# Optimization experiments

Measured on AMD Instinct MI355X. Metric: run time of the kernel, lower is better.

## Reference

```python
import jax, jax.numpy as jnp
import numpy as np
from jax import lax

S = 1024   # max_num_segments
CB = 25    # color_hist_bins
TB = 10    # texture_hist_bins
EPS = 1e-12


def setup_inputs() -> dict:
    key = jax.random.key(0)
    k1, k2, k3, k4 = jax.random.split(key, 4)
    B, C, R, H, W = 8, 3, 8, 512, 512
    img = jax.random.normal(k1, (B, C, H, W), jnp.float32)
    imgs_bins = jax.random.randint(k2, (B, C, H, W), 0, CB, jnp.int32)
    grads_bins = jax.random.randint(k3, (B, C, R, H, W), 0, TB, jnp.int32)
    reg_lab = jax.random.randint(k4, (B, H, W), 0, S, jnp.int32)
    return {"img": img, "imgs_bins": imgs_bins, "grads_bins": grads_bins, "reg_lab": reg_lab}


def reference(img, imgs_bins, grads_bins, reg_lab):
    B, C, H, W = img.shape
    R = grads_bins.shape[2]
    HW = H * W
    lab = reg_lab.astype(jnp.int32)

    # ---- area_per_segment: scatter_add of ones over flattened labels ----
    flat = (lab.reshape(B, HW) + (jnp.arange(B, dtype=jnp.int32) * S)[:, None]).reshape(-1)
    area = jnp.zeros(B * S, jnp.int32).at[flat].add(1).reshape(B, S)

    # ---- bbox_per_segment: scatter amin/amax of pixel coordinates ----
    yy, xx = jnp.meshgrid(jnp.arange(H, dtype=jnp.int32),
                          jnp.arange(W, dtype=jnp.int32), indexing='ij')
    xb = jnp.broadcast_to(xx.reshape(HW), (B, HW)).reshape(-1)
    yb = jnp.broadcast_to(yy.reshape(HW), (B, HW)).reshape(-1)
    xmin = jnp.full(B * S, W, jnp.int32).at[flat].min(xb)
    ymin = jnp.full(B * S, H, jnp.int32).at[flat].min(yb)
    xmax = jnp.zeros(B * S, jnp.int32).at[flat].max(xb)
    ymax = jnp.zeros(B * S, jnp.int32).at[flat].max(yb)
    # torch does xywh[2:] -= xywh[:2] (no +1), so w = xmax - xmin
    bbox_xywh = jnp.stack([xmin, ymin, xmax - xmin, ymax - ymin], -1).reshape(B, S, 4)

    area_f = area.astype(jnp.float32)

    # ---- color histogram: scatter_add of ones into [B,C,S*CB] ----
    ci = (lab[:, None, :, :] * CB + imgs_bins).reshape(B * C, HW)
    ci = (ci + (jnp.arange(B * C, dtype=jnp.int32) * (S * CB))[:, None]).reshape(-1)
    color_hist = jnp.zeros(B * C * S * CB, jnp.float32).at[ci].add(1.0).reshape(B, C, S, CB)
    color_hist = color_hist.transpose(0, 2, 1, 3).reshape(B, S, C * CB)  # [B,S,C*CB]
    color_hist = color_hist / (area_f * float(C) + EPS)[..., None]

    # ---- texture histogram: scatter_add of ones into [B,C,R,S*TB] ----
    ti = (lab[:, None, None, :, :] * TB + grads_bins).reshape(B * C * R, HW)
    ti = (ti + (jnp.arange(B * C * R, dtype=jnp.int32) * (S * TB))[:, None]).reshape(-1)
    texture_hist = jnp.zeros(B * C * R * S * TB, jnp.float32).at[ti].add(1.0).reshape(B, C, R, S, TB)
    texture_hist = texture_hist.transpose(0, 3, 1, 2, 4).reshape(B, S, C * R * TB)  # [B,S,C*R*TB]
    texture_hist = texture_hist / (area_f * float(C * R) + EPS)[..., None]

    # ---- image_scharr_gradients: depthwise-style conv2d, padding=1 ----
    sx = jnp.array([[-3., 0., 3.], [-10., 0., 10.], [-3., 0., 3.]], jnp.float32)
    kern = jnp.stack([sx, sx.T])[:, None]  # [2,1,3,3]
    grads = lax.conv_general_dilated(img.reshape(B * C, 1, H, W), kern, (1, 1), 'SAME',
                                     dimension_numbers=('NCHW', 'OIHW', 'NCHW'))
    grads = grads.reshape(B, C, 2, H, W)

    return area, bbox_xywh, color_hist, texture_hist, grads
```

## Files before the change

kernel.cpp:

```cpp
#include <hip/hip_runtime.h>

#define B_ 8
#define C_ 3
#define R_ 8
#define H_ 512
#define W_ 512
#define HW_ (H_*W_)
#define S_ 1024
#define CB_ 25
#define TB_ 10

#define O_AREA 0
#define O_BBOX 8192
#define O_COLOR 40960
#define O_TEX 655360
#define O_GRADS 2621440

#define NBBOX 8
#define NTEX (B_*C_*R_)
#define NCOL (B_*C_)
#define NHIST (NBBOX + NTEX + NCOL)
#define NCONV 1024
#define NGRID (NHIST + NCONV)

__global__ __launch_bounds__(1024) void k_fused(
    const float* __restrict__ img,
    const int* __restrict__ imgs_bins,
    const int* __restrict__ grads_bins,
    const int* __restrict__ lab,
    float* __restrict__ out) {
  __shared__ unsigned smem[12800];
  const int bid = blockIdx.x;
  const int tid = threadIdx.x;

  if (bid < NBBOX) {
    const int b = bid;
    int* mn = (int*)smem;
    for (int i = tid; i < S_; i += 1024) {
      mn[i] = W_; mn[S_ + i] = H_; mn[2*S_ + i] = 0; mn[3*S_ + i] = 0;
    }
    __syncthreads();
    const int4* lp = (const int4*)(lab + (size_t)b * HW_);
    for (int t = tid; t < HW_/4; t += 1024) {
      const int4 lv = lp[t];
      const int p = t * 4;
      const int y = p >> 9;
      const int x = p & (W_ - 1);
      atomicMin(&mn[lv.x], x);       atomicMin(&mn[S_ + lv.x], y);
      atomicMax(&mn[2*S_ + lv.x], x);   atomicMax(&mn[3*S_ + lv.x], y);
      atomicMin(&mn[lv.y], x + 1);   atomicMin(&mn[S_ + lv.y], y);
      atomicMax(&mn[2*S_ + lv.y], x + 1); atomicMax(&mn[3*S_ + lv.y], y);
      atomicMin(&mn[lv.z], x + 2);   atomicMin(&mn[S_ + lv.z], y);
      atomicMax(&mn[2*S_ + lv.z], x + 2); atomicMax(&mn[3*S_ + lv.z], y);
      atomicMin(&mn[lv.w], x + 3);   atomicMin(&mn[S_ + lv.w], y);
      atomicMax(&mn[2*S_ + lv.w], x + 3); atomicMax(&mn[3*S_ + lv.w], y);
    }
    __syncthreads();
    {
      const int xmn = mn[tid], ymn = mn[S_ + tid];
      const int xmx = mn[2*S_ + tid], ymx = mn[3*S_ + tid];
      float4 v;
      v.x = (float)xmn; v.y = (float)ymn;
      v.z = (float)(xmx - xmn); v.w = (float)(ymx - ymn);
      ((float4*)(out + O_BBOX))[b * S_ + tid] = v;
    }
  } else if (bid < NBBOX + NTEX) {
    const int plane = bid - NBBOX;
    const int b = plane / (C_*R_);
    const int cr = plane - b * (C_*R_);
    int* h = (int*)smem;
    for (int i = tid; i < S_*TB_; i += 1024) h[i] = 0;
    __syncthreads();
    const int4* bp = (const int4*)(grads_bins + (size_t)plane * HW_);
    const int4* lp = (const int4*)(lab + (size_t)b * HW_);
    for (int t = tid; t < HW_/4; t += 1024) {
      const int4 bn = bp[t];
      const int4 lv = lp[t];
      atomicAdd(&h[lv.x*TB_ + bn.x], 1);
      atomicAdd(&h[lv.y*TB_ + bn.y], 1);
      atomicAdd(&h[lv.z*TB_ + bn.z], 1);
      atomicAdd(&h[lv.w*TB_ + bn.w], 1);
    }
    __syncthreads();
    {
      const int base = tid * TB_;
      int s = 0;
      #pragma unroll
      for (int t = 0; t < TB_; ++t) s += h[base + t];
      const float inv = 1.0f / ((float)s * 24.0f + 1e-12f);
      float* o = out + O_TEX + (size_t)b * (S_ * C_*R_*TB_) + tid * (C_*R_*TB_) + cr * TB_;
      #pragma unroll
      for (int t = 0; t < TB_; ++t) o[t] = (float)h[base + t] * inv;
      if (cr == 0) out[O_AREA + b * S_ + tid] = (float)s;
    }
  } else if (bid < NHIST) {
    const int plane = bid - NBBOX - NTEX;
    const int b = plane / C_;
    const int c = plane - b * C_;
    unsigned* h = smem;
    for (int i = tid; i < (S_*CB_)/2; i += 1024) h[i] = 0;
    __syncthreads();
    const int4* bp = (const int4*)(imgs_bins + (size_t)plane * HW_);
    const int4* lp = (const int4*)(lab + (size_t)b * HW_);
    for (int t = tid; t < HW_/4; t += 1024) {
      const int4 bn = bp[t];
      const int4 lv = lp[t];
      const int j0 = lv.x*CB_ + bn.x;
      const int j1 = lv.y*CB_ + bn.y;
      const int j2 = lv.z*CB_ + bn.z;
      const int j3 = lv.w*CB_ + bn.w;
      atomicAdd(&h[j0 >> 1], 1u << ((j0 & 1) << 4));
      atomicAdd(&h[j1 >> 1], 1u << ((j1 & 1) << 4));
      atomicAdd(&h[j2 >> 1], 1u << ((j2 & 1) << 4));
      atomicAdd(&h[j3 >> 1], 1u << ((j3 & 1) << 4));
    }
    __syncthreads();
    {
      int s = 0;
      #pragma unroll
      for (int ci = 0; ci < CB_; ++ci) {
        const int j = tid * CB_ + ci;
        s += (int)((h[j >> 1] >> ((j & 1) << 4)) & 0xFFFFu);
      }
      const float inv = 1.0f / ((float)s * 3.0f + 1e-12f);
      float* o = out + O_COLOR + (size_t)b * (S_ * C_*CB_) + tid * (C_*CB_) + c * CB_;
      #pragma unroll
      for (int ci = 0; ci < CB_; ++ci) {
        const int j = tid * CB_ + ci;
        o[ci] = (float)((h[j >> 1] >> ((j & 1) << 4)) & 0xFFFFu) * inv;
      }
    }
  } else {
    const int cb = bid - NHIST;
    const int tot = B_*C_*HW_;
    for (int i = cb * 1024 + tid; i < tot; i += NCONV * 1024) {
      const int pix = i & (HW_ - 1);
      const int bc = i >> 18;
      const int x = pix & (W_ - 1);
      const int y = pix >> 9;
      const float* im = img + (size_t)bc * HW_;
      const bool xm = x > 0, xp = x < W_ - 1, ym = y > 0, yp = y < H_ - 1;
      const float i00 = (ym && xm) ? im[pix - W_ - 1] : 0.f;
      const float i01 = ym ? im[pix - W_] : 0.f;
      const float i02 = (ym && xp) ? im[pix - W_ + 1] : 0.f;
      const float i10 = xm ? im[pix - 1] : 0.f;
      const float i12 = xp ? im[pix + 1] : 0.f;
      const float i20 = (yp && xm) ? im[pix + W_ - 1] : 0.f;
      const float i21 = yp ? im[pix + W_] : 0.f;
      const float i22 = (yp && xp) ? im[pix + W_ + 1] : 0.f;
      const float gx = 3.f*(i02 - i00) + 10.f*(i12 - i10) + 3.f*(i22 - i20);
      const float gy = 3.f*(i20 - i00) + 10.f*(i21 - i01) + 3.f*(i22 - i02);
      out[O_GRADS + (size_t)(bc*2 + 0)*HW_ + pix] = gx;
      out[O_GRADS + (size_t)(bc*2 + 1)*HW_ + pix] = gy;
    }
  }
}

extern "C" void kernel_launch(void* const* d_in, const int* in_sizes, int n_in,
                              void* d_out, int out_size, void* d_ws, size_t ws_size,
                              hipStream_t stream) {
  const float* img = (const float*)d_in[0];
  const int* imgs_bins = (const int*)d_in[1];
  const int* grads_bins = (const int*)d_in[2];
  const int* reg_lab = (const int*)d_in[3];
  float* out = (float*)d_out;

  hipLaunchKernelGGL(k_fused, dim3(NGRID), dim3(1024), 0, stream,
                     img, imgs_bins, grads_bins, reg_lab, out);
}
```

Measured before the change: 78.12 us.

## Split histogram planes into chunks with scratch partials and separate reduce kernel

```diff
diff --git a/kernel.cpp b/kernel.cpp
--- a/kernel.cpp
+++ b/kernel.cpp
@@ -16,64 +16,69 @@
 #define O_TEX 655360
 #define O_GRADS 2621440
 
-#define NBBOX 8
-#define NTEX (B_*C_*R_)
-#define NCOL (B_*C_)
-#define NHIST (NBBOX + NTEX + NCOL)
-#define NCONV 1024
-#define NGRID (NHIST + NCONV)
-
-__global__ __launch_bounds__(1024) void k_fused(
+#define NTEX 768
+#define NCOL 96
+#define NBB  128
+#define NAREA 8
+#define NHIST (NTEX + NCOL + NBB + NAREA)
+#define NCONV 512
+#define NGRID1 (NHIST + NCONV)
+
+#define SC_TEX 0
+#define SC_COL (NTEX * 5120)
+#define SC_B   (SC_COL + NCOL * 12800)
+#define SCR_WORDS (SC_B + NBB * 2048)
+#define NEED_WS ((size_t)SCR_WORDS * 4)
+
+#define T_TEX (B_*C_*R_*S_*TB_)
+#define T_COL (B_*C_*S_*CB_)
+#define T_BB  (B_*S_)
+#define NGRID2 ((T_TEX + T_COL + T_BB) / 1024)
+
+__device__ __forceinline__ void conv_px(const float* __restrict__ img,
+                                        float* __restrict__ out, int i) {
+  const int pix = i & (HW_ - 1);
+  const int bc = i >> 18;
+  const int x = pix & (W_ - 1);
+  const int y = pix >> 9;
+  const float* im = img + (size_t)bc * HW_;
+  const bool xm = x > 0, xp = x < W_ - 1, ym = y > 0, yp = y < H_ - 1;
+  const float i00 = (ym && xm) ? im[pix - W_ - 1] : 0.f;
+  const float i01 = ym ? im[pix - W_] : 0.f;
+  const float i02 = (ym && xp) ? im[pix - W_ + 1] : 0.f;
+  const float i10 = xm ? im[pix - 1] : 0.f;
+  const float i12 = xp ? im[pix + 1] : 0.f;
+  const float i20 = (yp && xm) ? im[pix + W_ - 1] : 0.f;
+  const float i21 = yp ? im[pix + W_] : 0.f;
+  const float i22 = (yp && xp) ? im[pix + W_ + 1] : 0.f;
+  const float gx = 3.f*(i02 - i00) + 10.f*(i12 - i10) + 3.f*(i22 - i20);
+  const float gy = 3.f*(i20 - i00) + 10.f*(i21 - i01) + 3.f*(i22 - i02);
+  out[O_GRADS + (size_t)(bc*2 + 0)*HW_ + pix] = gx;
+  out[O_GRADS + (size_t)(bc*2 + 1)*HW_ + pix] = gy;
+}
+
+__global__ __launch_bounds__(1024) void k_part(
     const float* __restrict__ img,
     const int* __restrict__ imgs_bins,
     const int* __restrict__ grads_bins,
     const int* __restrict__ lab,
-    float* __restrict__ out) {
+    float* __restrict__ out,
+    unsigned* __restrict__ scr,
+    int pxsplit) {
   __shared__ unsigned smem[12800];
   const int bid = blockIdx.x;
   const int tid = threadIdx.x;
 
-  if (bid < NBBOX) {
-    const int b = bid;
-    int* mn = (int*)smem;
-    for (int i = tid; i < S_; i += 1024) {
-      mn[i] = W_; mn[S_ + i] = H_; mn[2*S_ + i] = 0; mn[3*S_ + i] = 0;
-    }
-    __syncthreads();
-    const int4* lp = (const int4*)(lab + (size_t)b * HW_);
-    for (int t = tid; t < HW_/4; t += 1024) {
-      const int4 lv = lp[t];
-      const int p = t * 4;
-      const int y = p >> 9;
-      const int x = p & (W_ - 1);
-      atomicMin(&mn[lv.x], x);       atomicMin(&mn[S_ + lv.x], y);
-      atomicMax(&mn[2*S_ + lv.x], x);   atomicMax(&mn[3*S_ + lv.x], y);
-      atomicMin(&mn[lv.y], x + 1);   atomicMin(&mn[S_ + lv.y], y);
-      atomicMax(&mn[2*S_ + lv.y], x + 1); atomicMax(&mn[3*S_ + lv.y], y);
-      atomicMin(&mn[lv.z], x + 2);   atomicMin(&mn[S_ + lv.z], y);
-      atomicMax(&mn[2*S_ + lv.z], x + 2); atomicMax(&mn[3*S_ + lv.z], y);
-      atomicMin(&mn[lv.w], x + 3);   atomicMin(&mn[S_ + lv.w], y);
-      atomicMax(&mn[2*S_ + lv.w], x + 3); atomicMax(&mn[3*S_ + lv.w], y);
-    }
-    __syncthreads();
-    {
-      const int xmn = mn[tid], ymn = mn[S_ + tid];
-      const int xmx = mn[2*S_ + tid], ymx = mn[3*S_ + tid];
-      float4 v;
-      v.x = (float)xmn; v.y = (float)ymn;
-      v.z = (float)(xmx - xmn); v.w = (float)(ymx - ymn);
-      ((float4*)(out + O_BBOX))[b * S_ + tid] = v;
-    }
-  } else if (bid < NBBOX + NTEX) {
-    const int plane = bid - NBBOX;
+  if (bid < NTEX) {
+    const int plane = bid >> 2, chunk = bid & 3;
     const int b = plane / (C_*R_);
-    const int cr = plane - b * (C_*R_);
     int* h = (int*)smem;
     for (int i = tid; i < S_*TB_; i += 1024) h[i] = 0;
     __syncthreads();
-    const int4* bp = (const int4*)(grads_bins + (size_t)plane * HW_);
-    const int4* lp = (const int4*)(lab + (size_t)b * HW_);
-    for (int t = tid; t < HW_/4; t += 1024) {
+    const int4* bp = (const int4*)(grads_bins + (size_t)plane*HW_) + chunk*16384;
+    const int4* lp = (const int4*)(lab + (size_t)b*HW_) + chunk*16384;
+    #pragma unroll 4
+    for (int t = tid; t < 16384; t += 1024) {
       const int4 bn = bp[t];
       const int4 lv = lp[t];
       atomicAdd(&h[lv.x*TB_ + bn.x], 1);
@@ -82,27 +87,23 @@
       atomicAdd(&h[lv.w*TB_ + bn.w], 1);
     }
     __syncthreads();
-    {
-      const int base = tid * TB_;
-      int s = 0;
-      #pragma unroll
-      for (int t = 0; t < TB_; ++t) s += h[base + t];
-      const float inv = 1.0f / ((float)s * 24.0f + 1e-12f);
-      float* o = out + O_TEX + (size_t)b * (S_ * C_*R_*TB_) + tid * (C_*R_*TB_) + cr * TB_;
-      #pragma unroll
-      for (int t = 0; t < TB_; ++t) o[t] = (float)h[base + t] * inv;
-      if (cr == 0) out[O_AREA + b * S_ + tid] = (float)s;
-    }
-  } else if (bid < NHIST) {
-    const int plane = bid - NBBOX - NTEX;
+    unsigned* dst = scr + SC_TEX + (size_t)bid * 5120;
+    const int2* h2 = (const int2*)h;
+    for (int i = tid; i < 5120; i += 1024) {
+      const int2 v = h2[i];
+      dst[i] = (unsigned)v.x | ((unsigned)v.y << 16);
+    }
+  } else if (bid < NTEX + NCOL) {
+    const int rid = bid - NTEX;
+    const int plane = rid >> 2, chunk = rid & 3;
     const int b = plane / C_;
-    const int c = plane - b * C_;
     unsigned* h = smem;
-    for (int i = tid; i < (S_*CB_)/2; i += 1024) h[i] = 0;
-    __syncthreads();
-    const int4* bp = (const int4*)(imgs_bins + (size_t)plane * HW_);
-    const int4* lp = (const int4*)(lab + (size_t)b * HW_);
-    for (int t = tid; t < HW_/4; t += 1024) {
+    for (int i = tid; i < 12800; i += 1024) h[i] = 0;
+    __syncthreads();
+    const int4* bp = (const int4*)(imgs_bins + (size_t)plane*HW_) + chunk*16384;
+    const int4* lp = (const int4*)(lab + (size_t)b*HW_) + chunk*16384;
+    #pragma unroll 4
+    for (int t = tid; t < 16384; t += 1024) {
       const int4 bn = bp[t];
       const int4 lv = lp[t];
       const int j0 = lv.x*CB_ + bn.x;
@@ -115,45 +116,114 @@
       atomicAdd(&h[j3 >> 1], 1u << ((j3 & 1) << 4));
     }
     __syncthreads();
-    {
-      int s = 0;
-      #pragma unroll
-      for (int ci = 0; ci < CB_; ++ci) {
-        const int j = tid * CB_ + ci;
-        s += (int)((h[j >> 1] >> ((j & 1) << 4)) & 0xFFFFu);
-      }
-      const float inv = 1.0f / ((float)s * 3.0f + 1e-12f);
-      float* o = out + O_COLOR + (size_t)b * (S_ * C_*CB_) + tid * (C_*CB_) + c * CB_;
-      #pragma unroll
-      for (int ci = 0; ci < CB_; ++ci) {
-        const int j = tid * CB_ + ci;
-        o[ci] = (float)((h[j >> 1] >> ((j & 1) << 4)) & 0xFFFFu) * inv;
-      }
-    }
+    unsigned* dst = scr + SC_COL + (size_t)rid * 12800;
+    for (int i = tid; i < 12800; i += 1024) dst[i] = h[i];
+  } else if (bid < NTEX + NCOL + NBB) {
+    const int rid = bid - NTEX - NCOL;
+    const int b = rid >> 4, chunk = rid & 15;
+    int* mn = (int*)smem;
+    for (int i = tid; i < 2048; i += 1024) mn[i] = 512;
+    for (int i = tid; i < 2048; i += 1024) mn[2048 + i] = 0;
+    __syncthreads();
+    const int base = chunk * 16384;
+    const int4* lp = (const int4*)(lab + (size_t)b*HW_) + chunk*4096;
+    #pragma unroll 2
+    for (int t = tid; t < 4096; t += 1024) {
+      const int4 lv = lp[t];
+      const int p = base + t*4;
+      const int y = p >> 9;
+      const int x = p & (W_ - 1);
+      atomicMin(&mn[lv.x], x);       atomicMin(&mn[1024 + lv.x], y);
+      atomicMax(&mn[2048 + lv.x], x);     atomicMax(&mn[3072 + lv.x], y);
+      atomicMin(&mn[lv.y], x + 1);   atomicMin(&mn[1024 + lv.y], y);
+      atomicMax(&mn[2048 + lv.y], x + 1); atomicMax(&mn[3072 + lv.y], y);
+      atomicMin(&mn[lv.z], x + 2);   atomicMin(&mn[1024 + lv.z], y);
+      atomicMax(&mn[2048 + lv.z], x + 2); atomicMax(&mn[3072 + lv.z], y);
+      atomicMin(&mn[lv.w], x + 3);   atomicMin(&mn[1024 + lv.w], y);
+      atomicMax(&mn[2048 + lv.w], x + 3); atomicMax(&mn[3072 + lv.w], y);
+    }
+    __syncthreads();
+    unsigned* dst = scr + SC_B + (size_t)rid * 2048;
+    dst[tid]        = (unsigned)mn[tid]        | ((unsigned)mn[1024 + tid] << 16);
+    dst[1024 + tid] = (unsigned)mn[2048 + tid] | ((unsigned)mn[3072 + tid] << 16);
+  } else if (bid < NHIST) {
+    const int b = bid - NTEX - NCOL - NBB;
+    int* cnt = (int*)smem;
+    cnt[tid] = 0;
+    __syncthreads();
+    const int4* lp = (const int4*)(lab + (size_t)b*HW_);
+    #pragma unroll 4
+    for (int t = tid; t < HW_/4; t += 1024) {
+      const int4 lv = lp[t];
+      atomicAdd(&cnt[lv.x], 1);
+      atomicAdd(&cnt[lv.y], 1);
+      atomicAdd(&cnt[lv.z], 1);
+      atomicAdd(&cnt[lv.w], 1);
+    }
+    __syncthreads();
+    out[O_AREA + b*S_ + tid] = (float)cnt[tid];
   } else {
     const int cb = bid - NHIST;
-    const int tot = B_*C_*HW_;
-    for (int i = cb * 1024 + tid; i < tot; i += NCONV * 1024) {
-      const int pix = i & (HW_ - 1);
-      const int bc = i >> 18;
-      const int x = pix & (W_ - 1);
-      const int y = pix >> 9;
-      const float* im = img + (size_t)bc * HW_;
-      const bool xm = x > 0, xp = x < W_ - 1, ym = y > 0, yp = y < H_ - 1;
-      const float i00 = (ym && xm) ? im[pix - W_ - 1] : 0.f;
-      const float i01 = ym ? im[pix - W_] : 0.f;
-      const float i02 = (ym && xp) ? im[pix - W_ + 1] : 0.f;
-      const float i10 = xm ? im[pix - 1] : 0.f;
-      const float i12 = xp ? im[pix + 1] : 0.f;
-      const float i20 = (yp && xm) ? im[pix + W_ - 1] : 0.f;
-      const float i21 = yp ? im[pix + W_] : 0.f;
-      const float i22 = (yp && xp) ? im[pix + W_ + 1] : 0.f;
-      const float gx = 3.f*(i02 - i00) + 10.f*(i12 - i10) + 3.f*(i22 - i20);
-      const float gy = 3.f*(i20 - i00) + 10.f*(i21 - i01) + 3.f*(i22 - i02);
-      out[O_GRADS + (size_t)(bc*2 + 0)*HW_ + pix] = gx;
-      out[O_GRADS + (size_t)(bc*2 + 1)*HW_ + pix] = gy;
-    }
+    for (int i = pxsplit + cb*1024 + tid; i < B_*C_*HW_; i += NCONV*1024)
+      conv_px(img, out, i);
   }
+}
+
+__global__ __launch_bounds__(1024) void k_reduce(float* __restrict__ out,
+                                                 const unsigned* __restrict__ scr) {
+  const int idx = blockIdx.x * 1024 + threadIdx.x;
+  if (idx < T_TEX) {
+    const int b = idx / 245760;
+    const int r1 = idx - b * 245760;
+    const int l = r1 / 240;
+    const int r2 = r1 - l * 240;
+    const int cr = r2 / 10;
+    const int t = r2 - cr * 10;
+    const int j = l * TB_ + t;
+    const unsigned sh = (j & 1) << 4;
+    const unsigned* p = scr + SC_TEX + (size_t)(b*(C_*R_) + cr) * 4 * 5120 + (j >> 1);
+    const unsigned s = ((p[0] >> sh) & 0xFFFFu) + ((p[5120] >> sh) & 0xFFFFu)
+                     + ((p[2*5120] >> sh) & 0xFFFFu) + ((p[3*5120] >> sh) & 0xFFFFu);
+    const float a = out[O_AREA + b*S_ + l];
+    out[O_TEX + idx] = (float)s / (a * 24.0f + 1e-12f);
+  } else if (idx < T_TEX + T_COL) {
+    const int o = idx - T_TEX;
+    const int b = o / 76800;
+    const int r1 = o - b * 76800;
+    const int l = r1 / 75;
+    const int r2 = r1 - l * 75;
+    const int c = r2 / 25;
+    const int ci = r2 - c * 25;
+    const int j = l * CB_ + ci;
+    const unsigned sh = (j & 1) << 4;
+    const unsigned* p = scr + SC_COL + (size_t)(b*C_ + c) * 4 * 12800 + (j >> 1);
+    const unsigned s = ((p[0] >> sh) & 0xFFFFu) + ((p[12800] >> sh) & 0xFFFFu)
+                     + ((p[2*12800] >> sh) & 0xFFFFu) + ((p[3*12800] >> sh) & 0xFFFFu);
+    const float a = out[O_AREA + b*S_ + l];
+    out[O_COLOR + o] = (float)s / (a * 3.0f + 1e-12f);
+  } else {
+    const int i = idx - T_TEX - T_COL;
+    const int b = i >> 10, l = i & (S_ - 1);
+    int xmn = W_, ymn = H_, xmx = 0, ymx = 0;
+    const unsigned* p = scr + SC_B + (size_t)(b*16) * 2048 + l;
+    #pragma unroll
+    for (int k = 0; k < 16; ++k) {
+      const unsigned w0 = p[k*2048];
+      const unsigned w1 = p[k*2048 + 1024];
+      xmn = min(xmn, (int)(w0 & 0xFFFFu)); ymn = min(ymn, (int)(w0 >> 16));
+      xmx = max(xmx, (int)(w1 & 0xFFFFu)); ymx = max(ymx, (int)(w1 >> 16));
+    }
+    float4 v;
+    v.x = (float)xmn; v.y = (float)ymn;
+    v.z = (float)(xmx - xmn); v.w = (float)(ymx - ymn);
+    ((float4*)(out + O_BBOX))[i] = v;
+  }
+}
+
+__global__ __launch_bounds__(1024) void k_conv_lo(const float* __restrict__ img,
+                                                  float* __restrict__ out, int pxsplit) {
+  for (int i = blockIdx.x*1024 + threadIdx.x; i < pxsplit; i += NCONV*1024)
+    conv_px(img, out, i);
 }
 
 extern "C" void kernel_launch(void* const* d_in, const int* in_sizes, int n_in,
@@ -165,6 +235,15 @@
   const int* reg_lab = (const int*)d_in[3];
   float* out = (float*)d_out;
 
-  hipLaunchKernelGGL(k_fused, dim3(NGRID), dim3(1024), 0, stream,
-                     img, imgs_bins, grads_bins, reg_lab, out);
-}
+  const bool ws_ok = ws_size >= NEED_WS;
+  unsigned* scr = ws_ok ? (unsigned*)d_ws : (unsigned*)(out + O_GRADS);
+  const int pxsplit = ws_ok ? 0 : 11 * HW_;
+
+  hipLaunchKernelGGL(k_part, dim3(NGRID1), dim3(1024), 0, stream,
+                     img, imgs_bins, grads_bins, reg_lab, out, scr, pxsplit);
+  hipLaunchKernelGGL(k_reduce, dim3(NGRID2), dim3(1024), 0, stream, out, scr);
+  if (!ws_ok) {
+    hipLaunchKernelGGL(k_conv_lo, dim3(NCONV), dim3(1024), 0, stream,
+                       img, out, pxsplit);
+  }
+}
```

Result: slower. 90.34 us (+15.6%).

## Split bbox reduction across 16 chunks per image with global atomic merge

Applied to the files above, without the earlier changes.

```diff
diff --git a/kernel.cpp b/kernel.cpp
--- a/kernel.cpp
+++ b/kernel.cpp
@@ -16,12 +16,20 @@
 #define O_TEX 655360
 #define O_GRADS 2621440
 
-#define NBBOX 8
 #define NTEX (B_*C_*R_)
 #define NCOL (B_*C_)
-#define NHIST (NBBOX + NTEX + NCOL)
+#define NBBC (B_*16)
+#define NHIST (NTEX + NCOL + NBBC)
 #define NCONV 1024
 #define NGRID (NHIST + NCONV)
+
+__global__ __launch_bounds__(1024) void k_init_bbox(float* __restrict__ out) {
+  const int i = blockIdx.x * 1024 + threadIdx.x;
+  if (i < B_*S_) {
+    int4* p = (int4*)(out + O_BBOX);
+    p[i] = make_int4(W_, H_, 0, 0);
+  }
+}
 
 __global__ __launch_bounds__(1024) void k_fused(
     const float* __restrict__ img,
@@ -33,39 +41,8 @@
   const int bid = blockIdx.x;
   const int tid = threadIdx.x;
 
-  if (bid < NBBOX) {
-    const int b = bid;
-    int* mn = (int*)smem;
-    for (int i = tid; i < S_; i += 1024) {
-      mn[i] = W_; mn[S_ + i] = H_; mn[2*S_ + i] = 0; mn[3*S_ + i] = 0;
-    }
-    __syncthreads();
-    const int4* lp = (const int4*)(lab + (size_t)b * HW_);
-    for (int t = tid; t < HW_/4; t += 1024) {
-      const int4 lv = lp[t];
-      const int p = t * 4;
-      const int y = p >> 9;
-      const int x = p & (W_ - 1);
-      atomicMin(&mn[lv.x], x);       atomicMin(&mn[S_ + lv.x], y);
-      atomicMax(&mn[2*S_ + lv.x], x);   atomicMax(&mn[3*S_ + lv.x], y);
-      atomicMin(&mn[lv.y], x + 1);   atomicMin(&mn[S_ + lv.y], y);
-      atomicMax(&mn[2*S_ + lv.y], x + 1); atomicMax(&mn[3*S_ + lv.y], y);
-      atomicMin(&mn[lv.z], x + 2);   atomicMin(&mn[S_ + lv.z], y);
-      atomicMax(&mn[2*S_ + lv.z], x + 2); atomicMax(&mn[3*S_ + lv.z], y);
-      atomicMin(&mn[lv.w], x + 3);   atomicMin(&mn[S_ + lv.w], y);
-      atomicMax(&mn[2*S_ + lv.w], x + 3); atomicMax(&mn[3*S_ + lv.w], y);
-    }
-    __syncthreads();
-    {
-      const int xmn = mn[tid], ymn = mn[S_ + tid];
-      const int xmx = mn[2*S_ + tid], ymx = mn[3*S_ + tid];
-      float4 v;
-      v.x = (float)xmn; v.y = (float)ymn;
-      v.z = (float)(xmx - xmn); v.w = (float)(ymx - ymn);
-      ((float4*)(out + O_BBOX))[b * S_ + tid] = v;
-    }
-  } else if (bid < NBBOX + NTEX) {
-    const int plane = bid - NBBOX;
+  if (bid < NTEX) {
+    const int plane = bid;
     const int b = plane / (C_*R_);
     const int cr = plane - b * (C_*R_);
     int* h = (int*)smem;
@@ -93,8 +70,8 @@
       for (int t = 0; t < TB_; ++t) o[t] = (float)h[base + t] * inv;
       if (cr == 0) out[O_AREA + b * S_ + tid] = (float)s;
     }
-  } else if (bid < NHIST) {
-    const int plane = bid - NBBOX - NTEX;
+  } else if (bid < NTEX + NCOL) {
+    const int plane = bid - NTEX;
     const int b = plane / C_;
     const int c = plane - b * C_;
     unsigned* h = smem;
@@ -130,6 +107,37 @@
         o[ci] = (float)((h[j >> 1] >> ((j & 1) << 4)) & 0xFFFFu) * inv;
       }
     }
+  } else if (bid < NHIST) {
+    const int rid = bid - NTEX - NCOL;
+    const int b = rid >> 4, chunk = rid & 15;
+    int* mn = (int*)smem;
+    mn[tid] = W_; mn[1024 + tid] = H_; mn[2048 + tid] = 0; mn[3072 + tid] = 0;
+    __syncthreads();
+    const int base = chunk * 16384;
+    const int4* lp = (const int4*)(lab + (size_t)b * HW_) + chunk * 4096;
+    #pragma unroll 2
+    for (int t = tid; t < 4096; t += 1024) {
+      const int4 lv = lp[t];
+      const int p = base + t * 4;
+      const int y = p >> 9;
+      const int x = p & (W_ - 1);
+      atomicMin(&mn[lv.x], x);       atomicMin(&mn[1024 + lv.x], y);
+      atomicMax(&mn[2048 + lv.x], x);     atomicMax(&mn[3072 + lv.x], y);
+      atomicMin(&mn[lv.y], x + 1);   atomicMin(&mn[1024 + lv.y], y);
+      atomicMax(&mn[2048 + lv.y], x + 1); atomicMax(&mn[3072 + lv.y], y);
+      atomicMin(&mn[lv.z], x + 2);   atomicMin(&mn[1024 + lv.z], y);
+      atomicMax(&mn[2048 + lv.z], x + 2); atomicMax(&mn[3072 + lv.z], y);
+      atomicMin(&mn[lv.w], x + 3);   atomicMin(&mn[1024 + lv.w], y);
+      atomicMax(&mn[2048 + lv.w], x + 3); atomicMax(&mn[3072 + lv.w], y);
+    }
+    __syncthreads();
+    {
+      int* gb = (int*)(out + O_BBOX) + (size_t)(b * S_ + tid) * 4;
+      atomicMin(&gb[0], mn[tid]);
+      atomicMin(&gb[1], mn[1024 + tid]);
+      atomicMax(&gb[2], mn[2048 + tid]);
+      atomicMax(&gb[3], mn[3072 + tid]);
+    }
   } else {
     const int cb = bid - NHIST;
     const int tot = B_*C_*HW_;
@@ -156,6 +164,17 @@
   }
 }
 
+__global__ __launch_bounds__(1024) void k_fin_bbox(float* __restrict__ out) {
+  const int i = blockIdx.x * 1024 + threadIdx.x;
+  if (i < B_*S_) {
+    const int4 v = ((const int4*)(out + O_BBOX))[i];
+    float4 f;
+    f.x = (float)v.x; f.y = (float)v.y;
+    f.z = (float)(v.z - v.x); f.w = (float)(v.w - v.y);
+    ((float4*)(out + O_BBOX))[i] = f;
+  }
+}
+
 extern "C" void kernel_launch(void* const* d_in, const int* in_sizes, int n_in,
                               void* d_out, int out_size, void* d_ws, size_t ws_size,
                               hipStream_t stream) {
@@ -165,6 +184,8 @@
   const int* reg_lab = (const int*)d_in[3];
   float* out = (float*)d_out;
 
+  hipLaunchKernelGGL(k_init_bbox, dim3(8), dim3(1024), 0, stream, out);
   hipLaunchKernelGGL(k_fused, dim3(NGRID), dim3(1024), 0, stream,
                      img, imgs_bins, grads_bins, reg_lab, out);
+  hipLaunchKernelGGL(k_fin_bbox, dim3(8), dim3(1024), 0, stream, out);
 }
```

Measured after the change: 87.04 us. 11.4% more time.

## Split histogram and bbox work into partial blocks with a separate reduce kernel

Applied to the files above, without the earlier changes.

```diff
diff --git a/kernel.cpp b/kernel.cpp
--- a/kernel.cpp
+++ b/kernel.cpp
@@ -16,144 +16,199 @@
 #define O_TEX 655360
 #define O_GRADS 2621440
 
-#define NBBOX 8
-#define NTEX (B_*C_*R_)
-#define NCOL (B_*C_)
-#define NHIST (NBBOX + NTEX + NCOL)
+#define NTEXU 384
+#define NCOLU 48
+#define NBBU  128
+#define NHIST (NTEXU + NCOLU + NBBU)
 #define NCONV 1024
-#define NGRID (NHIST + NCONV)
-
-__global__ __launch_bounds__(1024) void k_fused(
+#define NGRID1 (NHIST + NCONV)
+
+#define SC_TEX 0
+#define SC_COL (NTEXU * 5120)
+#define SC_B   (SC_COL + NCOLU * 12800)
+#define SCR_WORDS (SC_B + NBBU * 2048)
+#define NEED_WS ((size_t)SCR_WORDS * 4)
+#define BCSKIP 6
+
+__device__ __forceinline__ void conv_px(const float* __restrict__ img,
+                                        float* __restrict__ out, int i) {
+  const int pix = i & (HW_ - 1);
+  const int bc = i >> 18;
+  const int x = pix & (W_ - 1);
+  const int y = pix >> 9;
+  const float* im = img + (size_t)bc * HW_;
+  const bool xm = x > 0, xp = x < W_ - 1, ym = y > 0, yp = y < H_ - 1;
+  const float i00 = (ym && xm) ? im[pix - W_ - 1] : 0.f;
+  const float i01 = ym ? im[pix - W_] : 0.f;
+  const float i02 = (ym && xp) ? im[pix - W_ + 1] : 0.f;
+  const float i10 = xm ? im[pix - 1] : 0.f;
+  const float i12 = xp ? im[pix + 1] : 0.f;
+  const float i20 = (yp && xm) ? im[pix + W_ - 1] : 0.f;
+  const float i21 = yp ? im[pix + W_] : 0.f;
+  const float i22 = (yp && xp) ? im[pix + W_ + 1] : 0.f;
+  const float gx = 3.f*(i02 - i00) + 10.f*(i12 - i10) + 3.f*(i22 - i20);
+  const float gy = 3.f*(i20 - i00) + 10.f*(i21 - i01) + 3.f*(i22 - i02);
+  out[O_GRADS + (size_t)(bc*2 + 0)*HW_ + pix] = gx;
+  out[O_GRADS + (size_t)(bc*2 + 1)*HW_ + pix] = gy;
+}
+
+__global__ __launch_bounds__(1024, 8) void k_part(
     const float* __restrict__ img,
     const int* __restrict__ imgs_bins,
     const int* __restrict__ grads_bins,
     const int* __restrict__ lab,
-    float* __restrict__ out) {
+    float* __restrict__ out,
+    unsigned* __restrict__ scr,
+    int convlo) {
   __shared__ unsigned smem[12800];
   const int bid = blockIdx.x;
   const int tid = threadIdx.x;
 
-  if (bid < NBBOX) {
-    const int b = bid;
+  if (bid < NTEXU) {
+    const int plane = bid >> 1, chunk = bid & 1;
+    const int b = plane / (C_*R_);
+    for (int i = tid; i < 5120; i += 1024) smem[i] = 0;
+    __syncthreads();
+    const int4* bp = (const int4*)(grads_bins + (size_t)plane*HW_) + chunk*32768;
+    const int4* lp = (const int4*)(lab + (size_t)b*HW_) + chunk*32768;
+    #pragma unroll 1
+    for (int it = 0; it < 8; ++it) {
+      const int i = it*4096 + tid;
+      const int4 b0 = bp[i], b1 = bp[i+1024], b2 = bp[i+2048], b3 = bp[i+3072];
+      const int4 l0 = lp[i], l1 = lp[i+1024], l2 = lp[i+2048], l3 = lp[i+3072];
+      #define TEX1(L,Bv) { const int j = (L)*TB_ + (Bv); \
+        atomicAdd(&smem[j >> 1], 1u << ((j & 1) << 4)); }
+      TEX1(l0.x,b0.x) TEX1(l0.y,b0.y) TEX1(l0.z,b0.z) TEX1(l0.w,b0.w)
+      TEX1(l1.x,b1.x) TEX1(l1.y,b1.y) TEX1(l1.z,b1.z) TEX1(l1.w,b1.w)
+      TEX1(l2.x,b2.x) TEX1(l2.y,b2.y) TEX1(l2.z,b2.z) TEX1(l2.w,b2.w)
+      TEX1(l3.x,b3.x) TEX1(l3.y,b3.y) TEX1(l3.z,b3.z) TEX1(l3.w,b3.w)
+      #undef TEX1
+    }
+    __syncthreads();
+    unsigned* dst = scr + SC_TEX + (size_t)bid * 5120;
+    for (int i = tid; i < 5120; i += 1024) dst[i] = smem[i];
+  } else if (bid < NTEXU + NCOLU) {
+    const int rid = bid - NTEXU;
+    const int plane = rid >> 1, chunk = rid & 1;
+    const int b = plane / C_;
+    for (int i = tid; i < 12800; i += 1024) smem[i] = 0;
+    __syncthreads();
+    const int4* bp = (const int4*)(imgs_bins + (size_t)plane*HW_) + chunk*32768;
+    const int4* lp = (const int4*)(lab + (size_t)b*HW_) + chunk*32768;
+    #pragma unroll 1
+    for (int it = 0; it < 8; ++it) {
+      const int i = it*4096 + tid;
+      const int4 b0 = bp[i], b1 = bp[i+1024], b2 = bp[i+2048], b3 = bp[i+3072];
+      const int4 l0 = lp[i], l1 = lp[i+1024], l2 = lp[i+2048], l3 = lp[i+3072];
+      #define COL1(L,Bv) { const int j = (L)*CB_ + (Bv); \
+        atomicAdd(&smem[j >> 1], 1u << ((j & 1) << 4)); }
+      COL1(l0.x,b0.x) COL1(l0.y,b0.y) COL1(l0.z,b0.z) COL1(l0.w,b0.w)
+      COL1(l1.x,b1.x) COL1(l1.y,b1.y) COL1(l1.z,b1.z) COL1(l1.w,b1.w)
+      COL1(l2.x,b2.x) COL1(l2.y,b2.y) COL1(l2.z,b2.z) COL1(l2.w,b2.w)
+      COL1(l3.x,b3.x) COL1(l3.y,b3.y) COL1(l3.z,b3.z) COL1(l3.w,b3.w)
+      #undef COL1
+    }
+    __syncthreads();
+    unsigned* dst = scr + SC_COL + (size_t)rid * 12800;
+    for (int i = tid; i < 12800; i += 1024) dst[i] = smem[i];
+  } else if (bid < NHIST) {
+    const int rid = bid - NTEXU - NCOLU;
+    const int b = rid >> 4, chunk = rid & 15;
     int* mn = (int*)smem;
-    for (int i = tid; i < S_; i += 1024) {
-      mn[i] = W_; mn[S_ + i] = H_; mn[2*S_ + i] = 0; mn[3*S_ + i] = 0;
-    }
-    __syncthreads();
-    const int4* lp = (const int4*)(lab + (size_t)b * HW_);
-    for (int t = tid; t < HW_/4; t += 1024) {
-      const int4 lv = lp[t];
-      const int p = t * 4;
-      const int y = p >> 9;
-      const int x = p & (W_ - 1);
-      atomicMin(&mn[lv.x], x);       atomicMin(&mn[S_ + lv.x], y);
-      atomicMax(&mn[2*S_ + lv.x], x);   atomicMax(&mn[3*S_ + lv.x], y);
-      atomicMin(&mn[lv.y], x + 1);   atomicMin(&mn[S_ + lv.y], y);
-      atomicMax(&mn[2*S_ + lv.y], x + 1); atomicMax(&mn[3*S_ + lv.y], y);
-      atomicMin(&mn[lv.z], x + 2);   atomicMin(&mn[S_ + lv.z], y);
-      atomicMax(&mn[2*S_ + lv.z], x + 2); atomicMax(&mn[3*S_ + lv.z], y);
-      atomicMin(&mn[lv.w], x + 3);   atomicMin(&mn[S_ + lv.w], y);
-      atomicMax(&mn[2*S_ + lv.w], x + 3); atomicMax(&mn[3*S_ + lv.w], y);
-    }
-    __syncthreads();
+    mn[tid] = W_; mn[1024+tid] = H_; mn[2048+tid] = 0; mn[3072+tid] = 0;
+    __syncthreads();
+    const int4* lp = (const int4*)(lab + (size_t)b*HW_) + chunk*4096;
     {
-      const int xmn = mn[tid], ymn = mn[S_ + tid];
-      const int xmx = mn[2*S_ + tid], ymx = mn[3*S_ + tid];
-      float4 v;
-      v.x = (float)xmn; v.y = (float)ymn;
-      v.z = (float)(xmx - xmn); v.w = (float)(ymx - ymn);
-      ((float4*)(out + O_BBOX))[b * S_ + tid] = v;
-    }
-  } else if (bid < NBBOX + NTEX) {
-    const int plane = bid - NBBOX;
-    const int b = plane / (C_*R_);
-    const int cr = plane - b * (C_*R_);
-    int* h = (int*)smem;
-    for (int i = tid; i < S_*TB_; i += 1024) h[i] = 0;
-    __syncthreads();
-    const int4* bp = (const int4*)(grads_bins + (size_t)plane * HW_);
-    const int4* lp = (const int4*)(lab + (size_t)b * HW_);
-    for (int t = tid; t < HW_/4; t += 1024) {
-      const int4 bn = bp[t];
-      const int4 lv = lp[t];
-      atomicAdd(&h[lv.x*TB_ + bn.x], 1);
-      atomicAdd(&h[lv.y*TB_ + bn.y], 1);
-      atomicAdd(&h[lv.z*TB_ + bn.z], 1);
-      atomicAdd(&h[lv.w*TB_ + bn.w], 1);
-    }
-    __syncthreads();
-    {
-      const int base = tid * TB_;
-      int s = 0;
-      #pragma unroll
-      for (int t = 0; t < TB_; ++t) s += h[base + t];
-      const float inv = 1.0f / ((float)s * 24.0f + 1e-12f);
-      float* o = out + O_TEX + (size_t)b * (S_ * C_*R_*TB_) + tid * (C_*R_*TB_) + cr * TB_;
-      #pragma unroll
-      for (int t = 0; t < TB_; ++t) o[t] = (float)h[base + t] * inv;
-      if (cr == 0) out[O_AREA + b * S_ + tid] = (float)s;
-    }
-  } else if (bid < NHIST) {
-    const int plane = bid - NBBOX - NTEX;
-    const int b = plane / C_;
-    const int c = plane - b * C_;
-    unsigned* h = smem;
-    for (int i = tid; i < (S_*CB_)/2; i += 1024) h[i] = 0;
-    __syncthreads();
-    const int4* bp = (const int4*)(imgs_bins + (size_t)plane * HW_);
-    const int4* lp = (const int4*)(lab + (size_t)b * HW_);
-    for (int t = tid; t < HW_/4; t += 1024) {
-      const int4 bn = bp[t];
-      const int4 lv = lp[t];
-      const int j0 = lv.x*CB_ + bn.x;
-      const int j1 = lv.y*CB_ + bn.y;
-      const int j2 = lv.z*CB_ + bn.z;
-      const int j3 = lv.w*CB_ + bn.w;
-      atomicAdd(&h[j0 >> 1], 1u << ((j0 & 1) << 4));
-      atomicAdd(&h[j1 >> 1], 1u << ((j1 & 1) << 4));
-      atomicAdd(&h[j2 >> 1], 1u << ((j2 & 1) << 4));
-      atomicAdd(&h[j3 >> 1], 1u << ((j3 & 1) << 4));
-    }
-    __syncthreads();
-    {
-      int s = 0;
-      #pragma unroll
-      for (int ci = 0; ci < CB_; ++ci) {
-        const int j = tid * CB_ + ci;
-        s += (int)((h[j >> 1] >> ((j & 1) << 4)) & 0xFFFFu);
-      }
-      const float inv = 1.0f / ((float)s * 3.0f + 1e-12f);
-      float* o = out + O_COLOR + (size_t)b * (S_ * C_*CB_) + tid * (C_*CB_) + c * CB_;
-      #pragma unroll
-      for (int ci = 0; ci < CB_; ++ci) {
-        const int j = tid * CB_ + ci;
-        o[ci] = (float)((h[j >> 1] >> ((j & 1) << 4)) & 0xFFFFu) * inv;
-      }
-    }
+      const int i = tid;
+      const int4 l0 = lp[i], l1 = lp[i+1024], l2 = lp[i+2048], l3 = lp[i+3072];
+      #define BB1(L,P) { const int y = (P) >> 9, x = (P) & (W_-1); \
+        atomicMin(&mn[L], x); atomicMin(&mn[1024+(L)], y); \
+        atomicMax(&mn[2048+(L)], x); atomicMax(&mn[3072+(L)], y); }
+      const int p0 = (chunk*4096 + tid) * 4;
+      BB1(l0.x, p0) BB1(l0.y, p0+1) BB1(l0.z, p0+2) BB1(l0.w, p0+3)
+      const int p1 = (chunk*4096 + 1024 + tid) * 4;
+      BB1(l1.x, p1) BB1(l1.y, p1+1) BB1(l1.z, p1+2) BB1(l1.w, p1+3)
+      const int p2 = (chunk*4096 + 2048 + tid) * 4;
+      BB1(l2.x, p2) BB1(l2.y, p2+1) BB1(l2.z, p2+2) BB1(l2.w, p2+3)
+      const int p3 = (chunk*4096 + 3072 + tid) * 4;
+      BB1(l3.x, p3) BB1(l3.y, p3+1) BB1(l3.z, p3+2) BB1(l3.w, p3+3)
+      #undef BB1
+    }
+    __syncthreads();
+    unsigned* dst = scr + SC_B + (size_t)rid * 2048;
+    dst[tid]      = (unsigned)mn[tid]      | ((unsigned)mn[1024+tid] << 16);
+    dst[1024+tid] = (unsigned)mn[2048+tid] | ((unsigned)mn[3072+tid] << 16);
   } else {
     const int cb = bid - NHIST;
-    const int tot = B_*C_*HW_;
-    for (int i = cb * 1024 + tid; i < tot; i += NCONV * 1024) {
-      const int pix = i & (HW_ - 1);
-      const int bc = i >> 18;
-      const int x = pix & (W_ - 1);
-      const int y = pix >> 9;
-      const float* im = img + (size_t)bc * HW_;
-      const bool xm = x > 0, xp = x < W_ - 1, ym = y > 0, yp = y < H_ - 1;
-      const float i00 = (ym && xm) ? im[pix - W_ - 1] : 0.f;
-      const float i01 = ym ? im[pix - W_] : 0.f;
-      const float i02 = (ym && xp) ? im[pix - W_ + 1] : 0.f;
-      const float i10 = xm ? im[pix - 1] : 0.f;
-      const float i12 = xp ? im[pix + 1] : 0.f;
-      const float i20 = (yp && xm) ? im[pix + W_ - 1] : 0.f;
-      const float i21 = yp ? im[pix + W_] : 0.f;
-      const float i22 = (yp && xp) ? im[pix + W_ + 1] : 0.f;
-      const float gx = 3.f*(i02 - i00) + 10.f*(i12 - i10) + 3.f*(i22 - i20);
-      const float gy = 3.f*(i20 - i00) + 10.f*(i21 - i01) + 3.f*(i22 - i02);
-      out[O_GRADS + (size_t)(bc*2 + 0)*HW_ + pix] = gx;
-      out[O_GRADS + (size_t)(bc*2 + 1)*HW_ + pix] = gy;
-    }
-  }
+    const int lo = convlo << 18;
+    for (int i = lo + cb*1024 + tid; i < (B_*C_) << 18; i += NCONV*1024)
+      conv_px(img, out, i);
+  }
+}
+
+__global__ __launch_bounds__(1024) void k_reduce(float* __restrict__ out,
+                                                 const unsigned* __restrict__ scr) {
+  __shared__ float aInv24[64], aInv3[64];
+  const int m = blockIdx.x;
+  const int b = m >> 4, l0 = (m & 15) * 64;
+  const int tid = threadIdx.x;
+  if (tid < 64) {
+    const int l = l0 + tid;
+    const unsigned* p0 = scr + SC_TEX + (size_t)(b*24*2 + 0)*5120 + l*5;
+    const unsigned* p1 = scr + SC_TEX + (size_t)(b*24*2 + 1)*5120 + l*5;
+    int s = 0;
+    #pragma unroll
+    for (int w = 0; w < 5; ++w) {
+      const unsigned a = p0[w], c = p1[w];
+      s += (int)(a & 0xFFFFu) + (int)(a >> 16) + (int)(c & 0xFFFFu) + (int)(c >> 16);
+    }
+    out[O_AREA + b*S_ + l] = (float)s;
+    aInv24[tid] = 1.0f / ((float)s * 24.0f + 1e-12f);
+    aInv3[tid]  = 1.0f / ((float)s * 3.0f + 1e-12f);
+  }
+  __syncthreads();
+  for (int k = tid; k < 64*240; k += 1024) {
+    const int dl = k / 240, rem = k - dl*240;
+    const int cr = rem / 10, t = rem - cr*10;
+    const int l = l0 + dl;
+    const int j = l*TB_ + t;
+    const unsigned sh = (j & 1) << 4;
+    const unsigned* p = scr + SC_TEX + (size_t)((b*24 + cr)*2)*5120 + (j >> 1);
+    const unsigned s = ((p[0] >> sh) & 0xFFFFu) + ((p[5120] >> sh) & 0xFFFFu);
+    out[O_TEX + (size_t)b*245760 + l*240 + rem] = (float)s * aInv24[dl];
+  }
+  for (int k = tid; k < 64*75; k += 1024) {
+    const int dl = k / 75, rem = k - dl*75;
+    const int c = rem / 25, ci = rem - c*25;
+    const int l = l0 + dl;
+    const int j = l*CB_ + ci;
+    const unsigned sh = (j & 1) << 4;
+    const unsigned* p = scr + SC_COL + (size_t)((b*3 + c)*2)*12800 + (j >> 1);
+    const unsigned s = ((p[0] >> sh) & 0xFFFFu) + ((p[12800] >> sh) & 0xFFFFu);
+    out[O_COLOR + (size_t)b*76800 + l*75 + rem] = (float)s * aInv3[dl];
+  }
+  if (tid < 64) {
+    const int l = l0 + tid;
+    int xmn = W_, ymn = H_, xmx = 0, ymx = 0;
+    const unsigned* p = scr + SC_B + (size_t)(b*16)*2048 + l;
+    #pragma unroll
+    for (int k = 0; k < 16; ++k) {
+      const unsigned w0 = p[k*2048];
+      const unsigned w1 = p[k*2048 + 1024];
+      xmn = min(xmn, (int)(w0 & 0xFFFFu)); ymn = min(ymn, (int)(w0 >> 16));
+      xmx = max(xmx, (int)(w1 & 0xFFFFu)); ymx = max(ymx, (int)(w1 >> 16));
+    }
+    float4 v;
+    v.x = (float)xmn; v.y = (float)ymn;
+    v.z = (float)(xmx - xmn); v.w = (float)(ymx - ymn);
+    ((float4*)(out + O_BBOX))[b*S_ + l] = v;
+  }
+}
+
+__global__ __launch_bounds__(1024) void k_conv_lo(const float* __restrict__ img,
+                                                  float* __restrict__ out) {
+  const int i = blockIdx.x*1024 + threadIdx.x;
+  conv_px(img, out, i);
 }
 
 extern "C" void kernel_launch(void* const* d_in, const int* in_sizes, int n_in,
@@ -165,6 +220,15 @@
   const int* reg_lab = (const int*)d_in[3];
   float* out = (float*)d_out;
 
-  hipLaunchKernelGGL(k_fused, dim3(NGRID), dim3(1024), 0, stream,
-                     img, imgs_bins, grads_bins, reg_lab, out);
-}
+  const bool ws_ok = ws_size >= NEED_WS;
+  unsigned* scr = ws_ok ? (unsigned*)d_ws : (unsigned*)(out + O_GRADS);
+  const int convlo = ws_ok ? 0 : BCSKIP;
+
+  hipLaunchKernelGGL(k_part, dim3(NGRID1), dim3(1024), 0, stream,
+                     img, imgs_bins, grads_bins, reg_lab, out, scr, convlo);
+  hipLaunchKernelGGL(k_reduce, dim3(128), dim3(1024), 0, stream, out, scr);
+  if (!ws_ok) {
+    hipLaunchKernelGGL(k_conv_lo, dim3((BCSKIP << 18) / 1024), dim3(1024), 0, stream,
+                       img, out);
+  }
+}
```

Result: slower. 85.03 us (+8.8%).
